# Kernel tuning notes

Hardware: AMD Instinct MI355X
Metric: run time of the kernel (lower is better)

## Reference

```python
import jax, jax.numpy as jnp
import numpy as np

DIM = 1024
NUM_HEADS = 16
DIM_HEAD = 64
POOL = 8  # int(sqrt(agent_num=64))
SCALE = DIM_HEAD ** -0.5


def setup_inputs() -> dict:
    key = jax.random.key(0)
    k1, k2, k3, k4 = jax.random.split(key, 4)
    inner = NUM_HEADS * DIM_HEAD
    x = jax.random.normal(k1, (4, 4096, DIM), dtype=jnp.float32)
    # qkv Linear (no bias): weight stored as (in, out) so forward is x @ Wqkv
    Wqkv = jax.random.normal(k2, (DIM, 3 * inner), dtype=jnp.float32) * (DIM ** -0.5)
    Wo = jax.random.normal(k3, (inner, DIM), dtype=jnp.float32) * (inner ** -0.5)
    bo = jax.random.normal(k4, (DIM,), dtype=jnp.float32) * 0.01
    return {"x": x, "Wqkv": Wqkv, "Wo": Wo, "bo": bo}


def reference(x, Wqkv, Wo, bo):
    b, t, _ = x.shape
    h, d = NUM_HEADS, DIM_HEAD
    qkv = x @ Wqkv                                   # [b, t, 3*h*d]
    qkv = qkv.reshape(b, t, 3, h, d)                 # split (qkv h d)
    qkv = jnp.transpose(qkv, (2, 0, 3, 1, 4))        # [3, b, h, t, d]
    q, k, v = qkv[0], qkv[1], qkv[2]
    # AdaptiveAvgPool2d((POOL, d)) on [b,h,t,d]: identity on d, mean-pool t -> POOL
    # (t divisible by POOL -> exact reshape+mean)
    agent = q.reshape(b, h, POOL, t // POOL, d).mean(axis=3)  # [b, h, P, d]
    # stage 1: agents attend over keys, aggregate values
    s1 = jnp.einsum('bhid,bhjd->bhij', agent * SCALE, k)      # [b, h, P, t]
    p1 = jax.nn.softmax(s1, axis=-1)
    v_agent = jnp.einsum('bhij,bhjd->bhid', p1, v)            # [b, h, P, d]
    # stage 2: queries attend over agent tokens
    s2 = jnp.einsum('bhid,bhjd->bhij', q * SCALE, agent)      # [b, h, t, P]
    p2 = jax.nn.softmax(s2, axis=-1)
    out = jnp.einsum('bhij,bhjd->bhid', p2, v_agent)          # [b, h, t, d]
    out = jnp.transpose(out, (0, 2, 1, 3)).reshape(b, t, h * d)
    return out @ Wo + bo
```

## Files before the change

### kernel.cpp

```cpp
#include <hip/hip_runtime.h>
#include <hip/hip_bf16.h>
#include <stdint.h>

typedef __bf16 bf16;
typedef __attribute__((ext_vector_type(8))) __bf16 bf16x8;
typedef __attribute__((ext_vector_type(2))) __bf16 bf16x2;
typedef __attribute__((ext_vector_type(4))) float f32x4;
typedef __attribute__((ext_vector_type(4))) unsigned int u32x4;

#define NH 16
#define DH 64
#define POOL 8
#define BATCH 4
#define SEQ 4096
#define DIMV 1024
#define QKV_N (3*DIMV)
#define M_TOTAL (BATCH*SEQ)
#define SCALE_F 0.125f
#define AGS_F (SCALE_F / 512.0f)
#define BH (BATCH*NH)
#define QKVSZ ((size_t)BH*SEQ*DH)
#define TCH 16
#define TCL (SEQ/TCH)
#define HP 128

#define AS1(p) ((const __attribute__((address_space(1))) void*)(p))
#define AS3(p) ((__attribute__((address_space(3))) void*)(p))
typedef const __attribute__((address_space(3))) char* lds_cp;

__global__ void convert_x(const float* __restrict__ in, bf16* __restrict__ out) {
  size_t i = ((size_t)blockIdx.x * 256 + threadIdx.x) * 8;
  float4 f0 = *(const float4*)(in + i);
  float4 f1 = *(const float4*)(in + i + 4);
  bf16x8 o;
  o[0] = (bf16)f0.x; o[1] = (bf16)f0.y; o[2] = (bf16)f0.z; o[3] = (bf16)f0.w;
  o[4] = (bf16)f1.x; o[5] = (bf16)f1.y; o[6] = (bf16)f1.z; o[7] = (bf16)f1.w;
  *(bf16x8*)(out + i) = o;
}

__global__ void transpose_f32_bf16(const float* __restrict__ in, bf16* __restrict__ out,
                                   int R, int C) {
  __shared__ float tile[32][33];
  int c0 = blockIdx.x * 32, r0 = blockIdx.y * 32;
  int tx = threadIdx.x & 31, ty = threadIdx.x >> 5;
  for (int i = ty; i < 32; i += 8)
    tile[i][tx] = in[(size_t)(r0 + i) * C + c0 + tx];
  __syncthreads();
  for (int i = ty; i < 32; i += 8)
    out[(size_t)(c0 + i) * R + r0 + tx] = (bf16)tile[tx][i];
}

__global__ __launch_bounds__(512, 2)
void gemm1_qkv(const bf16* __restrict__ A, const bf16* __restrict__ B,
               bf16* __restrict__ qkvOut, float* __restrict__ agentSum) {
  constexpr int K1 = DIMV;
  constexpr int NI = K1 / 128;

  __shared__ __align__(16) bf16 LA[2][2][8192];
  __shared__ __align__(16) bf16 LB[2][2][8192];

  const int tid  = threadIdx.x;
  const int w    = tid >> 6;
  const int lane = tid & 63;
  const int wm = (w >> 2) * 128;
  const int wn = (w & 3) * 64;

  const int bid = blockIdx.x;
  const int swz = (bid & 7) * 96 + (bid >> 3);
  const int m0 = (swz / 12) * 256;
  const int n0 = (swz % 12) * 256;

  const int rT  = tid >> 3;
  const int csT = (((tid & 7) ^ (rT & 7)) << 3);
  const bf16* Ag = A + (size_t)(m0 + rT) * K1 + csT;
  const bf16* Bg = B + (size_t)(n0 + rT) * K1 + csT;

  const int rA = lane & 15, C = lane >> 4, xr = rA & 7;
  const unsigned s0 = (unsigned)(((0 * 4 + C) ^ xr) << 4);
  const unsigned s1 = (unsigned)(((1 * 4 + C) ^ xr) << 4);
  const unsigned aoff = (unsigned)((wm + rA) << 7);
  const unsigned boff = (unsigned)((wn + rA) << 7);

  f32x4 acc[8][4] = {};
  u32x4 aR[4][2], bR[4][2];

#define STG(arr, Gp, half, kofs) do {                                         \
    const bf16* _s = (Gp) + (size_t)((half) * 128) * K1 + (kofs);             \
    char* _d = (char*)&arr[half][0] + (w << 10);                              \
    __builtin_amdgcn_global_load_lds(AS1(_s), AS3(_d), 16, 0, 0);             \
    __builtin_amdgcn_global_load_lds(AS1(_s + 64 * K1), AS3(_d + 8192), 16, 0, 0); \
  } while (0)

#define DSR0(d, p)    asm volatile("ds_read_b128 %0, %1" : "=v"(d) : "v"(p))
#define DSR(d, p, o)  asm volatile("ds_read_b128 %0, %1 offset:" o : "=v"(d) : "v"(p))

#define READS_A(LAb, qm) do {                                                 \
    lds_cp _p0 = (lds_cp)(const char*)&LAb[0][0] + aoff + s0 + (qm) * 8192;   \
    lds_cp _p1 = (lds_cp)(const char*)&LAb[0][0] + aoff + s1 + (qm) * 8192;   \
    DSR0(aR[0][0], _p0); DSR(aR[1][0], _p0, "2048");                          \
    DSR(aR[2][0], _p0, "4096"); DSR(aR[3][0], _p0, "6144");                   \
    DSR0(aR[0][1], _p1); DSR(aR[1][1], _p1, "2048");                          \
    DSR(aR[2][1], _p1, "4096"); DSR(aR[3][1], _p1, "6144");                   \
  } while (0)

#define READS_B01(LBb) do {                                                   \
    lds_cp _p0 = (lds_cp)(const char*)&LBb[0][0] + boff + s0;                 \
    lds_cp _p1 = (lds_cp)(const char*)&LBb[0][0] + boff + s1;                 \
    DSR0(bR[0][0], _p0); DSR(bR[1][0], _p0, "2048");                          \
    DSR0(bR[0][1], _p1); DSR(bR[1][1], _p1, "2048");                          \
  } while (0)

#define READS_B23(LBb) do {                                                   \
    lds_cp _p0 = (lds_cp)(const char*)&LBb[0][0] + boff + s0;                 \
    lds_cp _p1 = (lds_cp)(const char*)&LBb[0][0] + boff + s1;                 \
    DSR(bR[2][0], _p0, "4096"); DSR(bR[3][0], _p0, "6144");                   \
    DSR(bR[2][1], _p1, "4096"); DSR(bR[3][1], _p1, "6144");                   \
  } while (0)

#define MFMA_Q(qm, qn) do {                                                   \
    asm volatile("s_waitcnt lgkmcnt(0)");                                     \
    __builtin_amdgcn_sched_barrier(0);                                        \
    __builtin_amdgcn_s_setprio(1);                                            \
    _Pragma("unroll")                                                         \
    for (int il = 0; il < 4; ++il)                                            \
      _Pragma("unroll")                                                       \
      for (int jj = 0; jj < 2; ++jj) {                                        \
        f32x4& ac = acc[(qm) * 4 + il][(qn) * 2 + jj];                        \
        ac = __builtin_amdgcn_mfma_f32_16x16x32_bf16(                         \
            __builtin_bit_cast(bf16x8, aR[il][0]),                            \
            __builtin_bit_cast(bf16x8, bR[(qn) * 2 + jj][0]), ac, 0, 0, 0);   \
        ac = __builtin_amdgcn_mfma_f32_16x16x32_bf16(                         \
            __builtin_bit_cast(bf16x8, aR[il][1]),                            \
            __builtin_bit_cast(bf16x8, bR[(qn) * 2 + jj][1]), ac, 0, 0, 0);   \
      }                                                                       \
    __builtin_amdgcn_s_setprio(0);                                            \
    __builtin_amdgcn_sched_barrier(0);                                        \
  } while (0)

#define BAR __builtin_amdgcn_s_barrier()

  STG(LA[0], Ag, 0, 0); STG(LA[0], Ag, 1, 0);
  STG(LB[0], Bg, 0, 0); STG(LB[0], Bg, 1, 0);
  STG(LB[1], Bg, 0, 64); STG(LB[1], Bg, 1, 64);
  asm volatile("s_waitcnt vmcnt(4)");
  __builtin_amdgcn_sched_barrier(0);
  BAR;

  int kk = 0;
  for (int i = 0; i < NI - 1; ++i, kk += 128) {
    READS_A(LA[0], 0); READS_B01(LB[0]);
    STG(LA[1], Ag, 0, kk + 64);
    BAR; MFMA_Q(0, 0); BAR;
    READS_B23(LB[0]);
    STG(LA[1], Ag, 1, kk + 64);
    BAR; MFMA_Q(0, 1); BAR;
    READS_A(LA[0], 1);
    STG(LB[0], Bg, 0, kk + 128);
    BAR; MFMA_Q(1, 0); BAR;
    STG(LB[0], Bg, 1, kk + 128);
    BAR; MFMA_Q(1, 1);
    asm volatile("s_waitcnt vmcnt(4)");
    __builtin_amdgcn_sched_barrier(0);
    BAR;
    READS_A(LA[1], 0); READS_B01(LB[1]);
    STG(LA[0], Ag, 0, kk + 128);
    BAR; MFMA_Q(0, 0); BAR;
    READS_B23(LB[1]);
    STG(LA[0], Ag, 1, kk + 128);
    BAR; MFMA_Q(0, 1); BAR;
    READS_A(LA[1], 1);
    STG(LB[1], Bg, 0, kk + 192);
    BAR; MFMA_Q(1, 0); BAR;
    STG(LB[1], Bg, 1, kk + 192);
    BAR; MFMA_Q(1, 1);
    asm volatile("s_waitcnt vmcnt(4)");
    __builtin_amdgcn_sched_barrier(0);
    BAR;
  }
  READS_A(LA[0], 0); READS_B01(LB[0]);
  STG(LA[1], Ag, 0, kk + 64);
  BAR; MFMA_Q(0, 0); BAR;
  READS_B23(LB[0]);
  STG(LA[1], Ag, 1, kk + 64);
  BAR; MFMA_Q(0, 1); BAR;
  READS_A(LA[0], 1);
  BAR; MFMA_Q(1, 0); BAR;
  MFMA_Q(1, 1);
  asm volatile("s_waitcnt vmcnt(0)");
  __builtin_amdgcn_sched_barrier(0);
  BAR;
  READS_A(LA[1], 0); READS_B01(LB[1]);
  BAR; MFMA_Q(0, 0); BAR;
  READS_B23(LB[1]);
  BAR; MFMA_Q(0, 1); BAR;
  READS_A(LA[1], 1);
  BAR; MFMA_Q(1, 0); BAR;
  MFMA_Q(1, 1);

#undef STG
#undef DSR0
#undef DSR
#undef READS_A
#undef READS_B01
#undef READS_B23
#undef MFMA_Q
#undef BAR

  const int cr = (lane >> 4) * 4;
  const int cc = lane & 15;
  const int ncol  = n0 + wn;
  const int which = ncol >> 10;
  const int hh    = (ncol >> 6) & 15;
  const int rowb  = m0 + wm;
  const int bb_   = rowb >> 12;
  const int tb    = rowb & 4095;
  bf16* Cp = qkvOut + (size_t)which * QKVSZ + (size_t)(bb_ * NH + hh) * SEQ * DH;
#pragma unroll
  for (int i = 0; i < 8; ++i)
#pragma unroll
    for (int j = 0; j < 4; ++j)
#pragma unroll
      for (int r = 0; r < 4; ++r)
        Cp[(size_t)(tb + i * 16 + cr + r) * DH + j * 16 + cc] = (bf16)acc[i][j][r];

  if (which == 0) {
    const int pp = tb >> 9;
    float* ag = agentSum + ((size_t)(bb_ * NH + hh) * POOL + pp) * DH;
#pragma unroll
    for (int j = 0; j < 4; ++j) {
      float s = 0.f;
#pragma unroll
      for (int i = 0; i < 8; ++i)
        s += acc[i][j][0] + acc[i][j][1] + acc[i][j][2] + acc[i][j][3];
      s += __shfl_xor(s, 16);
      s += __shfl_xor(s, 32);
      if (lane < 16) atomicAdd(&ag[j * 16 + lane], s);
    }
  }
}

template <int MODE>
__global__ __launch_bounds__(256)
void gemm_bt(const bf16* __restrict__ A, const bf16* __restrict__ B,
             void* __restrict__ Cv, const float* __restrict__ bias,
             float* __restrict__ agentSum, int M, int N, int K) {
  __shared__ bf16 As[128 * 32];
  __shared__ bf16 Bs[128 * 32];
  const int tid  = threadIdx.x;
  const int w    = tid >> 6;
  const int lane = tid & 63;
  const int m0 = blockIdx.y * 128, n0 = blockIdx.x * 128;
  const int wm = (w & 1) * 64, wn = (w >> 1) * 64;

  const bf16* Bb = (MODE == 2) ? (B + (size_t)(m0 >> 12) * N * K) : B;

  f32x4 acc[4][4] = {};

  const int g0  = w * 2;
  const int rig = lane >> 2;
  const int kcs = (lane & 3) ^ ((rig >> 1) & 3);
  const bf16* Ap0 = A + (size_t)(m0 + g0 * 16 + rig) * K + kcs * 8;
  const bf16* Ap1 = Ap0 + (size_t)16 * K;
  const bf16* Bp0 = Bb + (size_t)(n0 + g0 * 16 + rig) * K + kcs * 8;
  const bf16* Bp1 = Bp0 + (size_t)16 * K;
  bf16* AsW0 = As + g0 * 512;
  bf16* AsW1 = As + (g0 + 1) * 512;
  bf16* BsW0 = Bs + g0 * 512;
  bf16* BsW1 = Bs + (g0 + 1) * 512;

  for (int k0 = 0; k0 < K; k0 += 32) {
    __syncthreads();
    __builtin_amdgcn_global_load_lds(AS1(Ap0 + k0), AS3(AsW0), 16, 0, 0);
    __builtin_amdgcn_global_load_lds(AS1(Ap1 + k0), AS3(AsW1), 16, 0, 0);
    __builtin_amdgcn_global_load_lds(AS1(Bp0 + k0), AS3(BsW0), 16, 0, 0);
    __builtin_amdgcn_global_load_lds(AS1(Bp1 + k0), AS3(BsW1), 16, 0, 0);
    __syncthreads();

    bf16x8 a[4], b[4];
    const int C = lane >> 4;
#pragma unroll
    for (int i = 0; i < 4; ++i) {
      int ar = wm + i * 16 + (lane & 15);
      int sw = C ^ ((ar >> 1) & 3);
      a[i] = *(const bf16x8*)&As[ar * 32 + sw * 8];
    }
#pragma unroll
    for (int j = 0; j < 4; ++j) {
      int br = wn + j * 16 + (lane & 15);
      int sw = C ^ ((br >> 1) & 3);
      b[j] = *(const bf16x8*)&Bs[br * 32 + sw * 8];
    }
#pragma unroll
    for (int i = 0; i < 4; ++i)
#pragma unroll
      for (int j = 0; j < 4; ++j)
        acc[i][j] = __builtin_amdgcn_mfma_f32_16x16x32_bf16(a[i], b[j], acc[i][j], 0, 0, 0);
  }

  const int cr = (lane >> 4) * 4;
  const int cc = lane & 15;
#pragma unroll
  for (int i = 0; i < 4; ++i) {
#pragma unroll
    for (int j = 0; j < 4; ++j) {
      int rowb = m0 + wm + i * 16 + cr;
      if (MODE == 2) {
        float* Cp = (float*)Cv;
        int col = n0 + wn + j * 16 + cc;
        float bb = bias[col];
#pragma unroll
        for (int r = 0; r < 4; ++r)
          Cp[(size_t)(rowb + r) * N + col] = acc[i][j][r] + bb;
      } else {
        bf16* Cp = (bf16*)Cv;
        int nbase = n0 + wn + j * 16;
        int which = nbase >> 10;
        int hh    = (nbase >> 6) & 15;
        int dd    = (nbase & 63) + cc;
        int bb_   = rowb >> 12;
#pragma unroll
        for (int r = 0; r < 4; ++r) {
          int t = (rowb + r) & 4095;
          size_t addr = (size_t)which * QKVSZ +
                        ((size_t)(bb_ * NH + hh) * SEQ + t) * DH + dd;
          Cp[addr] = (bf16)acc[i][j][r];
        }
      }
    }
  }
}

__global__ __launch_bounds__(256)
void stage1_fused(const bf16* __restrict__ k, const bf16* __restrict__ v,
                  const float* __restrict__ agentSum,
                  float* __restrict__ pm, float* __restrict__ pl,
                  float* __restrict__ pva) {
  const int tc = blockIdx.x, bh = blockIdx.y;
  const int tid = threadIdx.x;
  const int t0 = tc * TCL;

  __shared__ float agT[64][8];
  __shared__ float se[TCL][9];
  __shared__ float rm[4][8], rl[4][8];
  __shared__ float pr[4][8][64];

  for (int i = tid; i < 512; i += 256) {
    int p = i >> 6, d = i & 63;
    agT[d][p] = agentSum[(size_t)bh * 512 + i] * AGS_F;
  }
  __syncthreads();

  const bf16* krow = k + ((size_t)bh * SEQ + t0 + tid) * DH;
  float sc[8] = {};
#pragma unroll
  for (int dc = 0; dc < 8; ++dc) {
    bf16x8 k8 = *(const bf16x8*)(krow + dc * 8);
#pragma unroll
    for (int e = 0; e < 8; ++e) {
      float kv = (float)k8[e];
      int d = dc * 8 + e;
      float4 a0 = *(const float4*)&agT[d][0];
      float4 a1 = *(const float4*)&agT[d][4];
      sc[0] += a0.x * kv; sc[1] += a0.y * kv; sc[2] += a0.z * kv; sc[3] += a0.w * kv;
      sc[4] += a1.x * kv; sc[5] += a1.y * kv; sc[6] += a1.z * kv; sc[7] += a1.w * kv;
    }
  }

  float mx[8];
#pragma unroll
  for (int p = 0; p < 8; ++p) mx[p] = sc[p];
#pragma unroll
  for (int o = 32; o; o >>= 1)
#pragma unroll
    for (int p = 0; p < 8; ++p) mx[p] = fmaxf(mx[p], __shfl_xor(mx[p], o));
  if ((tid & 63) == 0)
#pragma unroll
    for (int p = 0; p < 8; ++p) rm[tid >> 6][p] = mx[p];
  __syncthreads();
  float m[8];
#pragma unroll
  for (int p = 0; p < 8; ++p)
    m[p] = fmaxf(fmaxf(rm[0][p], rm[1][p]), fmaxf(rm[2][p], rm[3][p]));

  float sl[8];
#pragma unroll
  for (int p = 0; p < 8; ++p) {
    float e = __expf(sc[p] - m[p]);
    se[tid][p] = e;
    sl[p] = e;
  }
#pragma unroll
  for (int o = 32; o; o >>= 1)
#pragma unroll
    for (int p = 0; p < 8; ++p) sl[p] += __shfl_xor(sl[p], o);
  if ((tid & 63) == 0)
#pragma unroll
    for (int p = 0; p < 8; ++p) rl[tid >> 6][p] = sl[p];
  __syncthreads();
  if (tid < 8) {
    float l = rl[0][tid] + rl[1][tid] + rl[2][tid] + rl[3][tid];
    pm[(size_t)(bh * TCH + tc) * 8 + tid] = m[tid];
    pl[(size_t)(bh * TCH + tc) * 8 + tid] = l;
  }

  const int p  = tid >> 5;
  const int dg = tid & 7;
  const int to = (tid >> 3) & 3;
  const bf16* vb = v + ((size_t)bh * SEQ + t0 + to) * DH + dg * 8;
  float a8[8] = {};
  for (int tl = to; tl < TCL; tl += 4) {
    float wgt = se[tl][p];
    bf16x8 v8 = *(const bf16x8*)(vb + (size_t)(tl - to) * DH);
#pragma unroll
    for (int e = 0; e < 8; ++e) a8[e] += wgt * (float)v8[e];
  }
#pragma unroll
  for (int e = 0; e < 8; ++e) pr[to][p][dg * 8 + e] = a8[e];
  __syncthreads();
  if (to == 0) {
    float* o = pva + ((size_t)(bh * TCH + tc) * 8 + p) * DH + dg * 8;
#pragma unroll
    for (int e = 0; e < 8; ++e)
      o[e] = pr[0][p][dg * 8 + e] + pr[1][p][dg * 8 + e] +
             pr[2][p][dg * 8 + e] + pr[3][p][dg * 8 + e];
  }
}

__global__ void combine_vag(const float* __restrict__ pm, const float* __restrict__ pl,
                            const float* __restrict__ pva, float* __restrict__ vag) {
  int bh = blockIdx.x;
#pragma unroll
  for (int e = threadIdx.x; e < 512; e += 256) {
    int p = e >> 6, d = e & 63;
    float M = -1e30f;
#pragma unroll
    for (int tc = 0; tc < TCH; ++tc)
      M = fmaxf(M, pm[(size_t)(bh * TCH + tc) * 8 + p]);
    float L = 0.f, acc = 0.f;
#pragma unroll
    for (int tc = 0; tc < TCH; ++tc) {
      float w = __expf(pm[(size_t)(bh * TCH + tc) * 8 + p] - M);
      L   += w * pl[(size_t)(bh * TCH + tc) * 8 + p];
      acc += w * pva[((size_t)(bh * TCH + tc) * 8 + p) * DH + d];
    }
    vag[(size_t)bh * 512 + e] = acc / L;
  }
}

__global__ void w2_build(const float* __restrict__ vag, const bf16* __restrict__ WoT,
                         bf16* __restrict__ W2T) {
  int b = blockIdx.y;
  int n = blockIdx.x * 16 + (threadIdx.x & 15);
  int h = threadIdx.x >> 4;
  __shared__ float vg[128][65];
  for (int i = threadIdx.x; i < 128 * 64; i += 256)
    vg[i >> 6][i & 63] = vag[(size_t)b * 128 * 64 + i];
  __syncthreads();
  float acc[8] = {};
  const bf16* wrow = WoT + (size_t)n * DIMV + h * 64;
#pragma unroll
  for (int dv = 0; dv < 8; ++dv) {
    bf16x8 wv = *(const bf16x8*)(wrow + dv * 8);
#pragma unroll
    for (int e = 0; e < 8; ++e) {
      float wf = (float)wv[e];
      int d = dv * 8 + e;
#pragma unroll
      for (int p = 0; p < 8; ++p) acc[p] += vg[h * 8 + p][d] * wf;
    }
  }
  bf16x8 o;
#pragma unroll
  for (int p = 0; p < 8; ++p) o[p] = (bf16)acc[p];
  *(bf16x8*)&W2T[((size_t)b * DIMV + n) * HP + h * 8] = o;
}

__global__ __launch_bounds__(256)
void p2_build(const bf16* __restrict__ q, const float* __restrict__ agentSum,
              bf16* __restrict__ P2) {
  const int bh = blockIdx.y;
  const int t  = blockIdx.x * 256 + threadIdx.x;
  const int tid = threadIdx.x;

  __shared__ float agT[64][8];
  for (int i = tid; i < 512; i += 256) {
    int p = i >> 6, d = i & 63;
    agT[d][p] = agentSum[(size_t)bh * 512 + i] * AGS_F;
  }
  __syncthreads();

  const bf16* qrow = q + ((size_t)bh * SEQ + t) * DH;
  float sc[8] = {};
#pragma unroll
  for (int dc = 0; dc < 8; ++dc) {
    bf16x8 q8 = *(const bf16x8*)(qrow + dc * 8);
#pragma unroll
    for (int e = 0; e < 8; ++e) {
      float qv = (float)q8[e];
      int d = dc * 8 + e;
      float4 a0 = *(const float4*)&agT[d][0];
      float4 a1 = *(const float4*)&agT[d][4];
      sc[0] += a0.x * qv; sc[1] += a0.y * qv; sc[2] += a0.z * qv; sc[3] += a0.w * qv;
      sc[4] += a1.x * qv; sc[5] += a1.y * qv; sc[6] += a1.z * qv; sc[7] += a1.w * qv;
    }
  }
  float m = sc[0];
#pragma unroll
  for (int p = 1; p < 8; ++p) m = fmaxf(m, sc[p]);
  float wsum = 0.f, wgt[8];
#pragma unroll
  for (int p = 0; p < 8; ++p) { wgt[p] = __expf(sc[p] - m); wsum += wgt[p]; }
  float inv = 1.0f / wsum;
  int b = bh >> 4, h = bh & 15;
  bf16x8 o8;
#pragma unroll
  for (int p = 0; p < 8; ++p) o8[p] = (bf16)(wgt[p] * inv);
  *(bf16x8*)&P2[((size_t)(b * SEQ + t)) * HP + h * 8] = o8;
}

extern "C" void kernel_launch(void* const* d_in, const int* in_sizes, int n_in,
                              void* d_out, int out_size, void* d_ws, size_t ws_size,
                              hipStream_t stream) {
  const float* x    = (const float*)d_in[0];
  const float* Wqkv = (const float*)d_in[1];
  const float* Wo   = (const float*)d_in[2];
  const float* bo   = (const float*)d_in[3];
  float* out = (float*)d_out;

  char* ws = (char*)d_ws;
  bf16* WqkvT = (bf16*)ws;                                   ws += (size_t)QKV_N * DIMV * 2;
  bf16* WoT   = (bf16*)ws;                                   ws += (size_t)DIMV * DIMV * 2;
  bf16* qkv   = (bf16*)ws;                                   ws += 3 * QKVSZ * 2;
  char* wsu   = ws;                                          ws += (size_t)M_TOTAL * DIMV * 2;
  bf16*  xb    = (bf16*)wsu;
  bf16*  P2    = (bf16*)wsu;
  bf16*  W2T   = (bf16*)(wsu + (size_t)M_TOTAL * HP * 2);
  float* agent = (float*)ws;                                 ws += 512 * 64 * 4;
  float* pm    = (float*)ws;                                 ws += BH * TCH * 8 * 4;
  float* pl    = (float*)ws;                                 ws += BH * TCH * 8 * 4;
  float* pva   = (float*)ws;                                 ws += (size_t)BH * TCH * 8 * DH * 4;
  float* vag   = (float*)ws;                                 ws += 512 * 64 * 4;

  const bf16* qp = qkv;
  const bf16* kp = qkv + QKVSZ;
  const bf16* vp = qkv + 2 * QKVSZ;

  hipMemsetAsync(agent, 0, 512 * 64 * 4, stream);

  convert_x<<<(size_t)M_TOTAL * DIMV / (256 * 8), 256, 0, stream>>>(x, xb);
  transpose_f32_bf16<<<dim3(QKV_N / 32, DIMV / 32), 256, 0, stream>>>(Wqkv, WqkvT, DIMV, QKV_N);
  transpose_f32_bf16<<<dim3(DIMV / 32, DIMV / 32), 256, 0, stream>>>(Wo, WoT, DIMV, DIMV);

  gemm1_qkv<<<768, 512, 0, stream>>>(xb, WqkvT, qkv, agent);

  p2_build<<<dim3(SEQ / 256, BH), 256, 0, stream>>>(qp, agent, P2);
  stage1_fused<<<dim3(TCH, BH), 256, 0, stream>>>(kp, vp, agent, pm, pl, pva);
  combine_vag<<<BH, 256, 0, stream>>>(pm, pl, pva, vag);
  w2_build<<<dim3(DIMV / 16, BATCH), 256, 0, stream>>>(vag, WoT, W2T);

  gemm_bt<2><<<dim3(DIMV / 128, M_TOTAL / 128), 256, 0, stream>>>(
      P2, W2T, (void*)out, bo, nullptr, M_TOTAL, DIMV, HP);
}
```

Before: 317.4 us.

## Restructure QKV GEMM main loop into register-double-buffered LDS pipeline

```diff
diff --git a/kernel.cpp b/kernel.cpp
--- a/kernel.cpp
+++ b/kernel.cpp
@@ -4,7 +4,6 @@
 
 typedef __bf16 bf16;
 typedef __attribute__((ext_vector_type(8))) __bf16 bf16x8;
-typedef __attribute__((ext_vector_type(2))) __bf16 bf16x2;
 typedef __attribute__((ext_vector_type(4))) float f32x4;
 typedef __attribute__((ext_vector_type(4))) unsigned int u32x4;
 
@@ -54,7 +53,7 @@
 void gemm1_qkv(const bf16* __restrict__ A, const bf16* __restrict__ B,
                bf16* __restrict__ qkvOut, float* __restrict__ agentSum) {
   constexpr int K1 = DIMV;
-  constexpr int NI = K1 / 128;
+  constexpr int NT = K1 / 64;
 
   __shared__ __align__(16) bf16 LA[2][2][8192];
   __shared__ __align__(16) bf16 LB[2][2][8192];
@@ -82,7 +81,7 @@
   const unsigned boff = (unsigned)((wn + rA) << 7);
 
   f32x4 acc[8][4] = {};
-  u32x4 aR[4][2], bR[4][2];
+  u32x4 aR[4][2], aR2[4][2], bR[4][2];
 
 #define STG(arr, Gp, half, kofs) do {                                         \
     const bf16* _s = (Gp) + (size_t)((half) * 128) * K1 + (kofs);             \
@@ -91,119 +90,99 @@
     __builtin_amdgcn_global_load_lds(AS1(_s + 64 * K1), AS3(_d + 8192), 16, 0, 0); \
   } while (0)
 
+#define STAGE(tt, bb) do { const int _k = (tt) * 64;                          \
+    STG(LA[bb], Ag, 0, _k); STG(LA[bb], Ag, 1, _k);                           \
+    STG(LB[bb], Bg, 0, _k); STG(LB[bb], Bg, 1, _k); } while (0)
+
 #define DSR0(d, p)    asm volatile("ds_read_b128 %0, %1" : "=v"(d) : "v"(p))
 #define DSR(d, p, o)  asm volatile("ds_read_b128 %0, %1 offset:" o : "=v"(d) : "v"(p))
 
-#define READS_A(LAb, qm) do {                                                 \
-    lds_cp _p0 = (lds_cp)(const char*)&LAb[0][0] + aoff + s0 + (qm) * 8192;   \
-    lds_cp _p1 = (lds_cp)(const char*)&LAb[0][0] + aoff + s1 + (qm) * 8192;   \
-    DSR0(aR[0][0], _p0); DSR(aR[1][0], _p0, "2048");                          \
-    DSR(aR[2][0], _p0, "4096"); DSR(aR[3][0], _p0, "6144");                   \
-    DSR0(aR[0][1], _p1); DSR(aR[1][1], _p1, "2048");                          \
-    DSR(aR[2][1], _p1, "4096"); DSR(aR[3][1], _p1, "6144");                   \
+#define ISSUE_A0(bb) do {                                                     \
+    lds_cp _pa0 = (lds_cp)(const char*)&LA[bb][0][0] + aoff + s0;             \
+    lds_cp _pa1 = (lds_cp)(const char*)&LA[bb][0][0] + aoff + s1;             \
+    DSR0(aR[0][0], _pa0); DSR(aR[1][0], _pa0, "2048");                        \
+    DSR(aR[2][0], _pa0, "4096"); DSR(aR[3][0], _pa0, "6144");                 \
+    DSR0(aR[0][1], _pa1); DSR(aR[1][1], _pa1, "2048");                        \
+    DSR(aR[2][1], _pa1, "4096"); DSR(aR[3][1], _pa1, "6144");                 \
   } while (0)
 
-#define READS_B01(LBb) do {                                                   \
-    lds_cp _p0 = (lds_cp)(const char*)&LBb[0][0] + boff + s0;                 \
-    lds_cp _p1 = (lds_cp)(const char*)&LBb[0][0] + boff + s1;                 \
-    DSR0(bR[0][0], _p0); DSR(bR[1][0], _p0, "2048");                          \
-    DSR0(bR[0][1], _p1); DSR(bR[1][1], _p1, "2048");                          \
+#define ISSUE_REST(bb) do {                                                   \
+    lds_cp _pb0 = (lds_cp)(const char*)&LB[bb][0][0] + boff + s0;             \
+    lds_cp _pb1 = (lds_cp)(const char*)&LB[bb][0][0] + boff + s1;             \
+    DSR0(bR[0][0], _pb0); DSR(bR[1][0], _pb0, "2048");                        \
+    DSR0(bR[0][1], _pb1); DSR(bR[1][1], _pb1, "2048");                        \
+    DSR(bR[2][0], _pb0, "4096"); DSR(bR[3][0], _pb0, "6144");                 \
+    DSR(bR[2][1], _pb1, "4096"); DSR(bR[3][1], _pb1, "6144");                 \
+    lds_cp _pa0 = (lds_cp)(const char*)&LA[bb][0][0] + aoff + s0 + 8192;      \
+    lds_cp _pa1 = (lds_cp)(const char*)&LA[bb][0][0] + aoff + s1 + 8192;      \
+    DSR0(aR2[0][0], _pa0); DSR(aR2[1][0], _pa0, "2048");                      \
+    DSR(aR2[2][0], _pa0, "4096"); DSR(aR2[3][0], _pa0, "6144");               \
+    DSR0(aR2[0][1], _pa1); DSR(aR2[1][1], _pa1, "2048");                      \
+    DSR(aR2[2][1], _pa1, "4096"); DSR(aR2[3][1], _pa1, "6144");               \
   } while (0)
 
-#define READS_B23(LBb) do {                                                   \
-    lds_cp _p0 = (lds_cp)(const char*)&LBb[0][0] + boff + s0;                 \
-    lds_cp _p1 = (lds_cp)(const char*)&LBb[0][0] + boff + s1;                 \
-    DSR(bR[2][0], _p0, "4096"); DSR(bR[3][0], _p0, "6144");                   \
-    DSR(bR[2][1], _p1, "4096"); DSR(bR[3][1], _p1, "6144");                   \
-  } while (0)
-
-#define MFMA_Q(qm, qn) do {                                                   \
-    asm volatile("s_waitcnt lgkmcnt(0)");                                     \
-    __builtin_amdgcn_sched_barrier(0);                                        \
-    __builtin_amdgcn_s_setprio(1);                                            \
+#define MFMA_G(AS, qm, qn) do {                                               \
+    __builtin_amdgcn_s_setprio(1);                                           \
     _Pragma("unroll")                                                         \
     for (int il = 0; il < 4; ++il)                                            \
       _Pragma("unroll")                                                       \
       for (int jj = 0; jj < 2; ++jj) {                                        \
         f32x4& ac = acc[(qm) * 4 + il][(qn) * 2 + jj];                        \
         ac = __builtin_amdgcn_mfma_f32_16x16x32_bf16(                         \
-            __builtin_bit_cast(bf16x8, aR[il][0]),                            \
+            __builtin_bit_cast(bf16x8, AS[il][0]),                            \
             __builtin_bit_cast(bf16x8, bR[(qn) * 2 + jj][0]), ac, 0, 0, 0);   \
         ac = __builtin_amdgcn_mfma_f32_16x16x32_bf16(                         \
-            __builtin_bit_cast(bf16x8, aR[il][1]),                            \
+            __builtin_bit_cast(bf16x8, AS[il][1]),                            \
             __builtin_bit_cast(bf16x8, bR[(qn) * 2 + jj][1]), ac, 0, 0, 0);   \
       }                                                                       \
-    __builtin_amdgcn_s_setprio(0);                                            \
-    __builtin_amdgcn_sched_barrier(0);                                        \
+    __builtin_amdgcn_s_setprio(0);                                           \
   } while (0)
 
+#define WAITL(n) do { asm volatile("s_waitcnt lgkmcnt(" #n ")");              \
+                      __builtin_amdgcn_sched_barrier(0); } while (0)
+#define WAITV0   do { asm volatile("s_waitcnt vmcnt(0)");                     \
+                      __builtin_amdgcn_sched_barrier(0); } while (0)
 #define BAR __builtin_amdgcn_s_barrier()
 
-  STG(LA[0], Ag, 0, 0); STG(LA[0], Ag, 1, 0);
-  STG(LB[0], Bg, 0, 0); STG(LB[0], Bg, 1, 0);
-  STG(LB[1], Bg, 0, 64); STG(LB[1], Bg, 1, 64);
-  asm volatile("s_waitcnt vmcnt(4)");
-  __builtin_amdgcn_sched_barrier(0);
+  STAGE(0, 0);
+  WAITV0;
   BAR;
-
-  int kk = 0;
-  for (int i = 0; i < NI - 1; ++i, kk += 128) {
-    READS_A(LA[0], 0); READS_B01(LB[0]);
-    STG(LA[1], Ag, 0, kk + 64);
-    BAR; MFMA_Q(0, 0); BAR;
-    READS_B23(LB[0]);
-    STG(LA[1], Ag, 1, kk + 64);
-    BAR; MFMA_Q(0, 1); BAR;
-    READS_A(LA[0], 1);
-    STG(LB[0], Bg, 0, kk + 128);
-    BAR; MFMA_Q(1, 0); BAR;
-    STG(LB[0], Bg, 1, kk + 128);
-    BAR; MFMA_Q(1, 1);
-    asm volatile("s_waitcnt vmcnt(4)");
-    __builtin_amdgcn_sched_barrier(0);
-    BAR;
-    READS_A(LA[1], 0); READS_B01(LB[1]);
-    STG(LA[0], Ag, 0, kk + 128);
-    BAR; MFMA_Q(0, 0); BAR;
-    READS_B23(LB[1]);
-    STG(LA[0], Ag, 1, kk + 128);
-    BAR; MFMA_Q(0, 1); BAR;
-    READS_A(LA[1], 1);
-    STG(LB[1], Bg, 0, kk + 192);
-    BAR; MFMA_Q(1, 0); BAR;
-    STG(LB[1], Bg, 1, kk + 192);
-    BAR; MFMA_Q(1, 1);
-    asm volatile("s_waitcnt vmcnt(4)");
-    __builtin_amdgcn_sched_barrier(0);
-    BAR;
-  }
-  READS_A(LA[0], 0); READS_B01(LB[0]);
-  STG(LA[1], Ag, 0, kk + 64);
-  BAR; MFMA_Q(0, 0); BAR;
-  READS_B23(LB[0]);
-  STG(LA[1], Ag, 1, kk + 64);
-  BAR; MFMA_Q(0, 1); BAR;
-  READS_A(LA[0], 1);
-  BAR; MFMA_Q(1, 0); BAR;
-  MFMA_Q(1, 1);
-  asm volatile("s_waitcnt vmcnt(0)");
-  __builtin_amdgcn_sched_barrier(0);
-  BAR;
-  READS_A(LA[1], 0); READS_B01(LB[1]);
-  BAR; MFMA_Q(0, 0); BAR;
-  READS_B23(LB[1]);
-  BAR; MFMA_Q(0, 1); BAR;
-  READS_A(LA[1], 1);
-  BAR; MFMA_Q(1, 0); BAR;
-  MFMA_Q(1, 1);
+  ISSUE_A0(0);
+  ISSUE_REST(0);
+  STAGE(1, 1);
+
+  for (int t = 0; t < NT; ++t) {
+    const int cur = t & 1, nxt = cur ^ 1;
+    WAITL(12);
+    MFMA_G(aR, 0, 0);
+    WAITL(8);
+    MFMA_G(aR, 0, 1);
+    if (t < NT - 1) {
+      WAITV0;
+      BAR;
+      ISSUE_A0(nxt);
+      WAITL(8);
+      MFMA_G(aR2, 1, 0);
+      MFMA_G(aR2, 1, 1);
+      BAR;
+      ISSUE_REST(nxt);
+      if (t < NT - 2) STAGE(t + 2, cur);
+    } else {
+      WAITL(0);
+      MFMA_G(aR2, 1, 0);
+      MFMA_G(aR2, 1, 1);
+    }
+  }
 
 #undef STG
+#undef STAGE
 #undef DSR0
 #undef DSR
-#undef READS_A
-#undef READS_B01
-#undef READS_B23
-#undef MFMA_Q
+#undef ISSUE_A0
+#undef ISSUE_REST
+#undef MFMA_G
+#undef WAITL
+#undef WAITV0
 #undef BAR
 
   const int cr = (lane >> 4) * 4;
```

Measured after the change: 327.3 us. 1.03x slower.

## Merge prep kernels and replace final GEMM with 256x256 hand-scheduled kernel

Applied to the files above, without the earlier changes.

```diff
diff --git a/kernel.cpp b/kernel.cpp
--- a/kernel.cpp
+++ b/kernel.cpp
@@ -4,7 +4,6 @@
 
 typedef __bf16 bf16;
 typedef __attribute__((ext_vector_type(8))) __bf16 bf16x8;
-typedef __attribute__((ext_vector_type(2))) __bf16 bf16x2;
 typedef __attribute__((ext_vector_type(4))) float f32x4;
 typedef __attribute__((ext_vector_type(4))) unsigned int u32x4;
 
@@ -28,20 +27,26 @@
 #define AS3(p) ((__attribute__((address_space(3))) void*)(p))
 typedef const __attribute__((address_space(3))) char* lds_cp;
 
-__global__ void convert_x(const float* __restrict__ in, bf16* __restrict__ out) {
-  size_t i = ((size_t)blockIdx.x * 256 + threadIdx.x) * 8;
-  float4 f0 = *(const float4*)(in + i);
-  float4 f1 = *(const float4*)(in + i + 4);
-  bf16x8 o;
-  o[0] = (bf16)f0.x; o[1] = (bf16)f0.y; o[2] = (bf16)f0.z; o[3] = (bf16)f0.w;
-  o[4] = (bf16)f1.x; o[5] = (bf16)f1.y; o[6] = (bf16)f1.z; o[7] = (bf16)f1.w;
-  *(bf16x8*)(out + i) = o;
-}
-
-__global__ void transpose_f32_bf16(const float* __restrict__ in, bf16* __restrict__ out,
-                                   int R, int C) {
+__global__ void prep(const float* __restrict__ x, bf16* __restrict__ xb,
+                     const float* __restrict__ Wqkv, bf16* __restrict__ WqkvT,
+                     const float* __restrict__ Wo, bf16* __restrict__ WoT) {
   __shared__ float tile[32][33];
-  int c0 = blockIdx.x * 32, r0 = blockIdx.y * 32;
+  const int b = blockIdx.x;
+  if (b < 8192) {
+    size_t i = ((size_t)b * 256 + threadIdx.x) * 8;
+    float4 f0 = *(const float4*)(x + i);
+    float4 f1 = *(const float4*)(x + i + 4);
+    bf16x8 o;
+    o[0] = (bf16)f0.x; o[1] = (bf16)f0.y; o[2] = (bf16)f0.z; o[3] = (bf16)f0.w;
+    o[4] = (bf16)f1.x; o[5] = (bf16)f1.y; o[6] = (bf16)f1.z; o[7] = (bf16)f1.w;
+    *(bf16x8*)(xb + i) = o;
+    return;
+  }
+  const float* in; bf16* out; int C, bx, by;
+  if (b < 8192 + 3072) { int bb = b - 8192;  in = Wqkv; out = WqkvT; C = QKV_N; bx = bb % 96; by = bb / 96; }
+  else                 { int bb = b - 11264; in = Wo;   out = WoT;   C = DIMV;  bx = bb % 32; by = bb / 32; }
+  const int R = DIMV;
+  int c0 = bx * 32, r0 = by * 32;
   int tx = threadIdx.x & 31, ty = threadIdx.x >> 5;
   for (int i = ty; i < 32; i += 8)
     tile[i][tx] = in[(size_t)(r0 + i) * C + c0 + tx];
@@ -239,95 +244,145 @@
   }
 }
 
-template <int MODE>
-__global__ __launch_bounds__(256)
-void gemm_bt(const bf16* __restrict__ A, const bf16* __restrict__ B,
-             void* __restrict__ Cv, const float* __restrict__ bias,
-             float* __restrict__ agentSum, int M, int N, int K) {
-  __shared__ bf16 As[128 * 32];
-  __shared__ bf16 Bs[128 * 32];
+__global__ __launch_bounds__(512, 2)
+void gemm2_256(const bf16* __restrict__ A, const bf16* __restrict__ B,
+               float* __restrict__ Out, const float* __restrict__ bias) {
+  constexpr int K2 = HP;
+
+  __shared__ __align__(16) bf16 LA[2][2][8192];
+  __shared__ __align__(16) bf16 LB[2][2][8192];
+
   const int tid  = threadIdx.x;
   const int w    = tid >> 6;
   const int lane = tid & 63;
-  const int m0 = blockIdx.y * 128, n0 = blockIdx.x * 128;
-  const int wm = (w & 1) * 64, wn = (w >> 1) * 64;
-
-  const bf16* Bb = (MODE == 2) ? (B + (size_t)(m0 >> 12) * N * K) : B;
-
-  f32x4 acc[4][4] = {};
-
-  const int g0  = w * 2;
-  const int rig = lane >> 2;
-  const int kcs = (lane & 3) ^ ((rig >> 1) & 3);
-  const bf16* Ap0 = A + (size_t)(m0 + g0 * 16 + rig) * K + kcs * 8;
-  const bf16* Ap1 = Ap0 + (size_t)16 * K;
-  const bf16* Bp0 = Bb + (size_t)(n0 + g0 * 16 + rig) * K + kcs * 8;
-  const bf16* Bp1 = Bp0 + (size_t)16 * K;
-  bf16* AsW0 = As + g0 * 512;
-  bf16* AsW1 = As + (g0 + 1) * 512;
-  bf16* BsW0 = Bs + g0 * 512;
-  bf16* BsW1 = Bs + (g0 + 1) * 512;
-
-  for (int k0 = 0; k0 < K; k0 += 32) {
-    __syncthreads();
-    __builtin_amdgcn_global_load_lds(AS1(Ap0 + k0), AS3(AsW0), 16, 0, 0);
-    __builtin_amdgcn_global_load_lds(AS1(Ap1 + k0), AS3(AsW1), 16, 0, 0);
-    __builtin_amdgcn_global_load_lds(AS1(Bp0 + k0), AS3(BsW0), 16, 0, 0);
-    __builtin_amdgcn_global_load_lds(AS1(Bp1 + k0), AS3(BsW1), 16, 0, 0);
-    __syncthreads();
-
-    bf16x8 a[4], b[4];
-    const int C = lane >> 4;
-#pragma unroll
-    for (int i = 0; i < 4; ++i) {
-      int ar = wm + i * 16 + (lane & 15);
-      int sw = C ^ ((ar >> 1) & 3);
-      a[i] = *(const bf16x8*)&As[ar * 32 + sw * 8];
-    }
-#pragma unroll
-    for (int j = 0; j < 4; ++j) {
-      int br = wn + j * 16 + (lane & 15);
-      int sw = C ^ ((br >> 1) & 3);
-      b[j] = *(const bf16x8*)&Bs[br * 32 + sw * 8];
-    }
-#pragma unroll
-    for (int i = 0; i < 4; ++i)
-#pragma unroll
-      for (int j = 0; j < 4; ++j)
-        acc[i][j] = __builtin_amdgcn_mfma_f32_16x16x32_bf16(a[i], b[j], acc[i][j], 0, 0, 0);
-  }
+  const int wm = (w >> 2) * 128;
+  const int wn = (w & 3) * 64;
+
+  const int bid = blockIdx.x;
+  const int swz = (bid & 7) * 32 + (bid >> 3);
+  const int m0 = (swz >> 2) * 256;
+  const int n0 = (swz & 3) * 256;
+
+  const int rT  = tid >> 3;
+  const int csT = (((tid & 7) ^ (rT & 7)) << 3);
+  const bf16* Ag = A + (size_t)(m0 + rT) * K2 + csT;
+  const bf16* Bg = B + ((size_t)(m0 >> 12) * DIMV + n0 + rT) * K2 + csT;
+
+  const int rA = lane & 15, C = lane >> 4, xr = rA & 7;
+  const unsigned s0 = (unsigned)(((0 * 4 + C) ^ xr) << 4);
+  const unsigned s1 = (unsigned)(((1 * 4 + C) ^ xr) << 4);
+  const unsigned aoff = (unsigned)((wm + rA) << 7);
+  const unsigned boff = (unsigned)((wn + rA) << 7);
+
+  f32x4 acc[8][4] = {};
+  u32x4 aR[4][2], bR[4][2];
+
+#define STG(arr, Gp, half, kofs) do {                                         \
+    const bf16* _s = (Gp) + (size_t)((half) * 128) * K2 + (kofs);             \
+    char* _d = (char*)&arr[half][0] + (w << 10);                              \
+    __builtin_amdgcn_global_load_lds(AS1(_s), AS3(_d), 16, 0, 0);             \
+    __builtin_amdgcn_global_load_lds(AS1(_s + 64 * K2), AS3(_d + 8192), 16, 0, 0); \
+  } while (0)
+
+#define DSR0(d, p)    asm volatile("ds_read_b128 %0, %1" : "=v"(d) : "v"(p))
+#define DSR(d, p, o)  asm volatile("ds_read_b128 %0, %1 offset:" o : "=v"(d) : "v"(p))
+
+#define READS_A(LAb, qm) do {                                                 \
+    lds_cp _p0 = (lds_cp)(const char*)&LAb[0][0] + aoff + s0 + (qm) * 8192;   \
+    lds_cp _p1 = (lds_cp)(const char*)&LAb[0][0] + aoff + s1 + (qm) * 8192;   \
+    DSR0(aR[0][0], _p0); DSR(aR[1][0], _p0, "2048");                          \
+    DSR(aR[2][0], _p0, "4096"); DSR(aR[3][0], _p0, "6144");                   \
+    DSR0(aR[0][1], _p1); DSR(aR[1][1], _p1, "2048");                          \
+    DSR(aR[2][1], _p1, "4096"); DSR(aR[3][1], _p1, "6144");                   \
+  } while (0)
+
+#define READS_B01(LBb) do {                                                   \
+    lds_cp _p0 = (lds_cp)(const char*)&LBb[0][0] + boff + s0;                 \
+    lds_cp _p1 = (lds_cp)(const char*)&LBb[0][0] + boff + s1;                 \
+    DSR0(bR[0][0], _p0); DSR(bR[1][0], _p0, "2048");                          \
+    DSR0(bR[0][1], _p1); DSR(bR[1][1], _p1, "2048");                          \
+  } while (0)
+
+#define READS_B23(LBb) do {                                                   \
+    lds_cp _p0 = (lds_cp)(const char*)&LBb[0][0] + boff + s0;                 \
+    lds_cp _p1 = (lds_cp)(const char*)&LBb[0][0] + boff + s1;                 \
+    DSR(bR[2][0], _p0, "4096"); DSR(bR[3][0], _p0, "6144");                   \
+    DSR(bR[2][1], _p1, "4096"); DSR(bR[3][1], _p1, "6144");                   \
+  } while (0)
+
+#define MFMA_Q(qm, qn) do {                                                   \
+    asm volatile("s_waitcnt lgkmcnt(0)");                                     \
+    __builtin_amdgcn_sched_barrier(0);                                        \
+    __builtin_amdgcn_s_setprio(1);                                            \
+    _Pragma("unroll")                                                         \
+    for (int il = 0; il < 4; ++il)                                            \
+      _Pragma("unroll")                                                       \
+      for (int jj = 0; jj < 2; ++jj) {                                        \
+        f32x4& ac = acc[(qm) * 4 + il][(qn) * 2 + jj];                        \
+        ac = __builtin_amdgcn_mfma_f32_16x16x32_bf16(                         \
+            __builtin_bit_cast(bf16x8, aR[il][0]),                            \
+            __builtin_bit_cast(bf16x8, bR[(qn) * 2 + jj][0]), ac, 0, 0, 0);   \
+        ac = __builtin_amdgcn_mfma_f32_16x16x32_bf16(                         \
+            __builtin_bit_cast(bf16x8, aR[il][1]),                            \
+            __builtin_bit_cast(bf16x8, bR[(qn) * 2 + jj][1]), ac, 0, 0, 0);   \
+      }                                                                       \
+    __builtin_amdgcn_s_setprio(0);                                            \
+    __builtin_amdgcn_sched_barrier(0);                                        \
+  } while (0)
+
+#define BAR __builtin_amdgcn_s_barrier()
+
+  STG(LA[0], Ag, 0, 0); STG(LA[0], Ag, 1, 0);
+  STG(LB[0], Bg, 0, 0); STG(LB[0], Bg, 1, 0);
+  STG(LB[1], Bg, 0, 64); STG(LB[1], Bg, 1, 64);
+  asm volatile("s_waitcnt vmcnt(4)");
+  __builtin_amdgcn_sched_barrier(0);
+  BAR;
+
+  READS_A(LA[0], 0); READS_B01(LB[0]);
+  STG(LA[1], Ag, 0, 64);
+  BAR; MFMA_Q(0, 0); BAR;
+  READS_B23(LB[0]);
+  STG(LA[1], Ag, 1, 64);
+  BAR; MFMA_Q(0, 1); BAR;
+  READS_A(LA[0], 1);
+  BAR; MFMA_Q(1, 0); BAR;
+  MFMA_Q(1, 1);
+  asm volatile("s_waitcnt vmcnt(0)");
+  __builtin_amdgcn_sched_barrier(0);
+  BAR;
+  READS_A(LA[1], 0); READS_B01(LB[1]);
+  BAR; MFMA_Q(0, 0); BAR;
+  READS_B23(LB[1]);
+  BAR; MFMA_Q(0, 1); BAR;
+  READS_A(LA[1], 1);
+  BAR; MFMA_Q(1, 0); BAR;
+  MFMA_Q(1, 1);
+
+#undef STG
+#undef DSR0
+#undef DSR
+#undef READS_A
+#undef READS_B01
+#undef READS_B23
+#undef MFMA_Q
+#undef BAR
 
   const int cr = (lane >> 4) * 4;
   const int cc = lane & 15;
-#pragma unroll
-  for (int i = 0; i < 4; ++i) {
+  const int rowb = m0 + wm;
+  float bb4[4];
+#pragma unroll
+  for (int j = 0; j < 4; ++j) bb4[j] = bias[n0 + wn + j * 16 + cc];
+#pragma unroll
+  for (int i = 0; i < 8; ++i)
 #pragma unroll
     for (int j = 0; j < 4; ++j) {
-      int rowb = m0 + wm + i * 16 + cr;
-      if (MODE == 2) {
-        float* Cp = (float*)Cv;
-        int col = n0 + wn + j * 16 + cc;
-        float bb = bias[col];
-#pragma unroll
-        for (int r = 0; r < 4; ++r)
-          Cp[(size_t)(rowb + r) * N + col] = acc[i][j][r] + bb;
-      } else {
-        bf16* Cp = (bf16*)Cv;
-        int nbase = n0 + wn + j * 16;
-        int which = nbase >> 10;
-        int hh    = (nbase >> 6) & 15;
-        int dd    = (nbase & 63) + cc;
-        int bb_   = rowb >> 12;
-#pragma unroll
-        for (int r = 0; r < 4; ++r) {
-          int t = (rowb + r) & 4095;
-          size_t addr = (size_t)which * QKVSZ +
-                        ((size_t)(bb_ * NH + hh) * SEQ + t) * DH + dd;
-          Cp[addr] = (bf16)acc[i][j][r];
-        }
-      }
+      const int col = n0 + wn + j * 16 + cc;
+#pragma unroll
+      for (int r = 0; r < 4; ++r)
+        Out[(size_t)(rowb + i * 16 + cr + r) * DIMV + col] = acc[i][j][r] + bb4[j];
     }
-  }
 }
 
 __global__ __launch_bounds__(256)
@@ -547,9 +602,7 @@
 
   hipMemsetAsync(agent, 0, 512 * 64 * 4, stream);
 
-  convert_x<<<(size_t)M_TOTAL * DIMV / (256 * 8), 256, 0, stream>>>(x, xb);
-  transpose_f32_bf16<<<dim3(QKV_N / 32, DIMV / 32), 256, 0, stream>>>(Wqkv, WqkvT, DIMV, QKV_N);
-  transpose_f32_bf16<<<dim3(DIMV / 32, DIMV / 32), 256, 0, stream>>>(Wo, WoT, DIMV, DIMV);
+  prep<<<12288, 256, 0, stream>>>(x, xb, Wqkv, WqkvT, Wo, WoT);
 
   gemm1_qkv<<<768, 512, 0, stream>>>(xb, WqkvT, qkv, agent);
 
@@ -558,6 +611,5 @@
   combine_vag<<<BH, 256, 0, stream>>>(pm, pl, pva, vag);
   w2_build<<<dim3(DIMV / 16, BATCH), 256, 0, stream>>>(vag, WoT, W2T);
 
-  gemm_bt<2><<<dim3(DIMV / 128, M_TOTAL / 128), 256, 0, stream>>>(
-      P2, W2T, (void*)out, bo, nullptr, M_TOTAL, DIMV, HP);
-}
+  gemm2_256<<<256, 512, 0, stream>>>(P2, W2T, out, bo);
+}
```

New measurement: 317.7 us. About the same (+0.1%).
